# Optimization experiments

Hardware: AMD Instinct MI355X
Metric: run time of the kernel (lower is better)

The kernel has to match this reference:

```python
import jax, jax.numpy as jnp
import numpy as np

B, T, C, H, M, R = 2, 2048, 768, 6, 3072, 320
D = C // H  # head_dim = 128


def setup_inputs() -> dict:
    key = jax.random.key(0)
    ks = jax.random.split(key, 11)
    s = 0.02
    return {
        "x": jax.random.normal(ks[0], (B, T, C), jnp.float32),
        "forward_memory": jax.random.normal(ks[1], (B, M, C), jnp.float32),
        "reverse_memory": jax.random.normal(ks[2], (B, R, C), jnp.float32),
        "ctrl": jax.random.uniform(ks[3], (5,), jnp.float32),
        "Wq": jax.random.normal(ks[4], (C, C), jnp.float32) * s,
        "Wk": jax.random.normal(ks[5], (C, C), jnp.float32) * s,
        "Wv": jax.random.normal(ks[6], (C, C), jnp.float32) * s,
        "Wo": jax.random.normal(ks[7], (C, C), jnp.float32) * s,
        "Wc": jax.random.normal(ks[8], (C, 5), jnp.float32) * 1e-4,  # ctrl_init_scale
        "Wg": jax.random.normal(ks[9], (H, C), jnp.float32) * s,
        "bg": jnp.full((H,), -1.0, jnp.float32),  # gate_bias_init
    }


def reference(x, forward_memory, reverse_memory, ctrl, Wq, Wk, Wv, Wo, Wc, Wg, bg):
    Bx, Tx, Cx = x.shape
    Hx = bg.shape[0]
    Dx = Cx // Hx
    # query with control-vector fusion (ctrl broadcast to every token)
    q = x @ Wq.T + ctrl @ Wc.T  # [B,T,C]
    # concat local tokens with forward+reverse memory, project K/V once
    kv_in = jnp.concatenate([x, forward_memory, reverse_memory], axis=1)  # [B,S,C]
    k = kv_in @ Wk.T
    v = kv_in @ Wv.T

    def heads(t):
        return t.reshape(Bx, -1, Hx, Dx).transpose(0, 2, 1, 3)  # [B,H,*,D]

    qh, kh, vh = heads(q), heads(k), heads(v)
    S = kh.shape[2]
    scores = jnp.einsum("bhtd,bhsd->bhts", qh, kh) * (Dx ** -0.5)
    # causal mask over local block only; memory columns always visible
    causal = jnp.triu(jnp.ones((Tx, Tx), bool), 1)
    mask = jnp.concatenate([causal, jnp.zeros((Tx, S - Tx), bool)], axis=1)
    scores = jnp.where(mask, jnp.float32(-1e30), scores)
    w = jax.nn.softmax(scores, axis=-1)  # [B,H,T,S]
    # split attention output into local and memory contributions
    local = jnp.einsum("bhts,bhsd->bhtd", w[..., :Tx], vh[:, :, :Tx])
    mem = jnp.einsum("bhts,bhsd->bhtd", w[..., Tx:], vh[:, :, Tx:])
    # per-head sigmoid gate on the memory path, computed from the fused query
    gate = jax.nn.sigmoid(q @ Wg.T + bg)  # [B,T,H]
    gate = gate.transpose(0, 2, 1)[..., None]  # [B,H,T,1]
    out = local + gate * mem
    out = out.transpose(0, 2, 1, 3).reshape(Bx, Tx, Cx)
    return out @ Wo.T
```

## Files before the change

kernel.cpp:

```cpp
#include <hip/hip_runtime.h>


typedef unsigned short u16;
typedef unsigned int   u32;
typedef __bf16 bf16x8 __attribute__((ext_vector_type(8)));
typedef float  f32x4  __attribute__((ext_vector_type(4)));

#define B_ 2
#define T_ 2048
#define C_ 768
#define H_ 6
#define D_ 128
#define M_ 3072
#define R_ 320
#define S_ 5440
#define BT_ 4096
#define BS_ 10880
#define NS_ 3
#define NMEM_ 53

#define GLDS(src, dst) __builtin_amdgcn_global_load_lds( \
    (const __attribute__((address_space(1))) void*)(src), \
    (__attribute__((address_space(3))) void*)(dst), 16, 0, 0)

__device__ __forceinline__ float b2f(u16 u) {
  union { u32 i; float f; } c; c.i = ((u32)u) << 16; return c.f;
}
__device__ __forceinline__ u16 f2b(float f) {
  union { float f; u32 i; } c; c.f = f;
  return (u16)((c.i + 0x7FFFu + ((c.i >> 16) & 1u)) >> 16);
}

__global__ __launch_bounds__(256) void k_cast4(const float* __restrict__ s0,
                                               const float* __restrict__ s1,
                                               const float* __restrict__ s2,
                                               const float* __restrict__ s3,
                                               u16* __restrict__ d0,
                                               u16* __restrict__ d1,
                                               u16* __restrict__ d2,
                                               u16* __restrict__ d3) {
  const float* src = (blockIdx.y == 0) ? s0 : (blockIdx.y == 1) ? s1
                   : (blockIdx.y == 2) ? s2 : s3;
  u16* dst = (blockIdx.y == 0) ? d0 : (blockIdx.y == 1) ? d1
           : (blockIdx.y == 2) ? d2 : d3;
  int i = (blockIdx.x * 256 + threadIdx.x) * 4;
  float4 v = *(const float4*)(src + i);
  u16 o[4] = { f2b(v.x), f2b(v.y), f2b(v.z), f2b(v.w) };
  *(ushort4*)(dst + i) = *(ushort4*)o;
}

__global__ __launch_bounds__(256) void k_concat(const float* __restrict__ x,
                                                const float* __restrict__ fm,
                                                const float* __restrict__ rm,
                                                u16* __restrict__ kv) {
  long long i = ((long long)blockIdx.x * 256 + threadIdx.x) * 8;
  if (i >= (long long)BS_ * C_) return;
  int row = (int)(i / C_);
  int col = (int)(i - (long long)row * C_);
  int b = row / S_, s = row - b * S_;
  const float* src;
  if (s < T_)           src = x  + (size_t)(b * T_ + s) * C_ + col;
  else if (s < T_ + M_) src = fm + (size_t)(b * M_ + (s - T_)) * C_ + col;
  else                  src = rm + (size_t)(b * R_ + (s - T_ - M_)) * C_ + col;
  float4 a0 = *(const float4*)src;
  float4 a1 = *(const float4*)(src + 4);
  u16 o[8] = { f2b(a0.x), f2b(a0.y), f2b(a0.z), f2b(a0.w),
               f2b(a1.x), f2b(a1.y), f2b(a1.z), f2b(a1.w) };
  *(uint4*)(kv + i) = *(uint4*)o;
}

template<bool F32OUT, bool QCBIAS>
__global__ __launch_bounds__(256) void k_gemm(const u16* __restrict__ A,
                                              const u16* __restrict__ W,
                                              const float* __restrict__ ctrl,
                                              const float* __restrict__ Wc,
                                              void* __restrict__ outv,
                                              int rows, int rowShift, int bstride) {
  __shared__ __align__(16) u16 As[3][128 * 32];
  __shared__ __align__(16) u16 Bs[3][128 * 32];
  const int t = threadIdx.x;
  const int lane = t & 63, wv = t >> 6;
  const int wr = (wv >> 1) * 64, wc = (wv & 1) * 64;
  const int fr = lane & 15, fq = lane >> 4;
  const int rowTile = blockIdx.x * 128;
  const int colTile = blockIdx.y * 128;

  f32x4 acc[4][4] = {};

  const int e0 = t * 8;
  const int e1 = (256 + t) * 8;
  const int r0 = e0 >> 5, c0 = e0 & 31;
  const int r1 = e1 >> 5, c1 = e1 & 31;

  int gr0 = rowTile + r0; if (gr0 >= rows) gr0 = rows - 1;
  int gr1 = rowTile + r1; if (gr1 >= rows) gr1 = rows - 1;
  const int msk = (1 << rowShift) - 1;
  const size_t pr0 = (size_t)(gr0 >> rowShift) * bstride + (gr0 & msk);
  const size_t pr1 = (size_t)(gr1 >> rowShift) * bstride + (gr1 & msk);
  const u16* gaB0 = A + pr0 * C_ + c0;
  const u16* gaB1 = A + pr1 * C_ + c1;
  const u16* gbB0 = W + (size_t)(colTile + r0) * C_ + c0;
  const u16* gbB1 = W + (size_t)(colTile + r1) * C_ + c1;
  const int aOff0 = (wv * 64) * 8, aOff1 = (256 + wv * 64) * 8;

#define STAGE_G(bi, kt) do { \
    GLDS(gaB0 + (kt), &As[bi][aOff0]); \
    GLDS(gaB1 + (kt), &As[bi][aOff1]); \
    GLDS(gbB0 + (kt), &Bs[bi][aOff0]); \
    GLDS(gbB1 + (kt), &Bs[bi][aOff1]); } while (0)

  STAGE_G(0, 0);
  STAGE_G(1, 32);
  int cur = 0;

  for (int kt = 0; kt < C_; kt += 32) {
    int nx2 = cur + 2; if (nx2 >= 3) nx2 -= 3;
    if (kt + 64 < C_) {
      STAGE_G(nx2, kt + 64);
      asm volatile("s_waitcnt vmcnt(8)" ::: "memory");
    } else if (kt + 32 < C_) {
      asm volatile("s_waitcnt vmcnt(4)" ::: "memory");
    } else {
      asm volatile("s_waitcnt vmcnt(0)" ::: "memory");
    }
    __builtin_amdgcn_s_barrier();

    bf16x8 af[4], bfr[4];
#pragma unroll
    for (int i = 0; i < 4; ++i) af[i]  = *(const bf16x8*)&As[cur][(wr + i * 16 + fr) * 32 + fq * 8];
#pragma unroll
    for (int i = 0; i < 4; ++i) bfr[i] = *(const bf16x8*)&Bs[cur][(wc + i * 16 + fr) * 32 + fq * 8];
#pragma unroll
    for (int mi = 0; mi < 4; ++mi)
#pragma unroll
      for (int ni = 0; ni < 4; ++ni)
        acc[mi][ni] = __builtin_amdgcn_mfma_f32_16x16x32_bf16(af[mi], bfr[ni], acc[mi][ni], 0, 0, 0);
    __builtin_amdgcn_s_barrier();
    cur = (cur == 2) ? 0 : cur + 1;
  }
#undef STAGE_G

#pragma unroll
  for (int mi = 0; mi < 4; ++mi) {
#pragma unroll
    for (int ni = 0; ni < 4; ++ni) {
      int cc = colTile + wc + ni * 16 + fr;
      float bb = 0.f;
      if (QCBIAS) {
#pragma unroll
        for (int j = 0; j < 5; ++j) bb += ctrl[j] * Wc[cc * 5 + j];
      }
#pragma unroll
      for (int j = 0; j < 4; ++j) {
        int rr = rowTile + wr + mi * 16 + fq * 4 + j;
        if (rr < rows) {
          float val = acc[mi][ni][j] + bb;
          if (F32OUT) ((float*)outv)[(size_t)rr * C_ + cc] = val;
          else        ((u16*)outv)[(size_t)rr * C_ + cc] = f2b(val);
        }
      }
    }
  }
}

__global__ __launch_bounds__(256, 2) void k_gemmKV(const u16* __restrict__ kvb,
                                                   const u16* __restrict__ Wk,
                                                   const u16* __restrict__ Wv,
                                                   u16* __restrict__ kb,
                                                   u16* __restrict__ vt) {
  __shared__ __align__(16) u16 As[2][128 * 32];
  __shared__ __align__(16) u16 Ks2[2][128 * 32];
  __shared__ __align__(16) u16 Vs2[2][128 * 32];
  const int t = threadIdx.x;
  const int lane = t & 63, wv = t >> 6;
  const int wr = (wv >> 1) * 64, wc = (wv & 1) * 64;
  const int fr = lane & 15, fq = lane >> 4;
  const int rowTile = blockIdx.x * 128;
  const int colTile = blockIdx.y * 128;

  f32x4 accK[4][4] = {};
  f32x4 accV[4][4] = {};

  const int e0 = t * 8;
  const int e1 = (256 + t) * 8;
  const int r0 = e0 >> 5, c0 = e0 & 31;
  const int r1 = e1 >> 5, c1 = e1 & 31;

  const u16* gaB0 = kvb + (size_t)(rowTile + r0) * C_ + c0;
  const u16* gaB1 = kvb + (size_t)(rowTile + r1) * C_ + c1;
  const u16* gkB0 = Wk + (size_t)(colTile + r0) * C_ + c0;
  const u16* gkB1 = Wk + (size_t)(colTile + r1) * C_ + c1;
  const u16* gvB0 = Wv + (size_t)(colTile + r0) * C_ + c0;
  const u16* gvB1 = Wv + (size_t)(colTile + r1) * C_ + c1;
  const int aOff0 = (wv * 64) * 8, aOff1 = (256 + wv * 64) * 8;

#define STAGE_KV(bi, kt) do { \
    GLDS(gaB0 + (kt), &As[bi][aOff0]); \
    GLDS(gaB1 + (kt), &As[bi][aOff1]); \
    GLDS(gkB0 + (kt), &Ks2[bi][aOff0]); \
    GLDS(gkB1 + (kt), &Ks2[bi][aOff1]); \
    GLDS(gvB0 + (kt), &Vs2[bi][aOff0]); \
    GLDS(gvB1 + (kt), &Vs2[bi][aOff1]); } while (0)

  STAGE_KV(0, 0);
  int cur = 0;

  for (int kt = 0; kt < C_; kt += 32) {
    if (kt + 32 < C_) {
      STAGE_KV(cur ^ 1, kt + 32);
      asm volatile("s_waitcnt vmcnt(6)" ::: "memory");
    } else {
      asm volatile("s_waitcnt vmcnt(0)" ::: "memory");
    }
    __builtin_amdgcn_s_barrier();

    bf16x8 af[4], wkf[4], wvf[4];
#pragma unroll
    for (int i = 0; i < 4; ++i) af[i]  = *(const bf16x8*)&As[cur][(wr + i * 16 + fr) * 32 + fq * 8];
#pragma unroll
    for (int i = 0; i < 4; ++i) wkf[i] = *(const bf16x8*)&Ks2[cur][(wc + i * 16 + fr) * 32 + fq * 8];
#pragma unroll
    for (int i = 0; i < 4; ++i) wvf[i] = *(const bf16x8*)&Vs2[cur][(wc + i * 16 + fr) * 32 + fq * 8];
#pragma unroll
    for (int mi = 0; mi < 4; ++mi)
#pragma unroll
      for (int ni = 0; ni < 4; ++ni) {
        accK[mi][ni] = __builtin_amdgcn_mfma_f32_16x16x32_bf16(af[mi], wkf[ni], accK[mi][ni], 0, 0, 0);
        accV[mi][ni] = __builtin_amdgcn_mfma_f32_16x16x32_bf16(wvf[mi], af[ni], accV[mi][ni], 0, 0, 0);
      }
    __builtin_amdgcn_s_barrier();
    cur ^= 1;
  }
#undef STAGE_KV

#pragma unroll
  for (int mi = 0; mi < 4; ++mi) {
#pragma unroll
    for (int ni = 0; ni < 4; ++ni) {
      int cc = colTile + wc + ni * 16 + fr;
#pragma unroll
      for (int j = 0; j < 4; ++j) {
        int rr = rowTile + wr + mi * 16 + fq * 4 + j;
        kb[(size_t)rr * C_ + cc] = f2b(accK[mi][ni][j]);
      }
    }
  }
#pragma unroll
  for (int mi = 0; mi < 4; ++mi) {
#pragma unroll
    for (int ni = 0; ni < 4; ++ni) {
      int sg = rowTile + wr + ni * 16 + fr;
      int b = sg / S_, s = sg - b * S_;
#pragma unroll
      for (int j = 0; j < 4; ++j) {
        int cc = colTile + wc + mi * 16 + fq * 4 + j;
        vt[((size_t)(b * C_ + cc)) * S_ + s] = f2b(accV[mi][ni][j]);
      }
    }
  }
}

__global__ __launch_bounds__(256) void k_gate(const u16* __restrict__ q,
                                              const float* __restrict__ Wg,
                                              const float* __restrict__ bg,
                                              float* __restrict__ gate) {
  int gid = blockIdx.x * 4 + (threadIdx.x >> 6);
  int lane = threadIdx.x & 63;
  int h = gid % H_;
  int bt = gid / H_;
  const u16* qrow = q + (size_t)bt * C_;
  const float* wrow = Wg + (size_t)h * C_;
  float a = 0.f;
#pragma unroll
  for (int i = 0; i < 12; ++i) {
    int e = i * 64 + lane;
    a += b2f(qrow[e]) * wrow[e];
  }
#pragma unroll
  for (int off = 1; off < 64; off <<= 1) a += __shfl_xor(a, off);
  if (lane == 0) {
    float xg = a + bg[h];
    int b = bt / T_, tt = bt - b * T_;
    gate[((size_t)b * H_ + h) * T_ + tt] = 1.f / (1.f + __expf(-xg));
  }
}

__global__ __launch_bounds__(512, 4) void k_attn6(const u16* __restrict__ q,
                                                  const u16* __restrict__ kk,
                                                  const u16* __restrict__ vt,
                                                  const float* __restrict__ gate,
                                                  u16* __restrict__ pacc0,
                                                  u16* __restrict__ pacc1,
                                                  u16* __restrict__ pacc2,
                                                  float* __restrict__ pl) {
  __shared__ __align__(16) u16 Ks[2][64 * 128];
  __shared__ __align__(16) u16 Vs[128 * 64];
  __shared__ __align__(16) u16 Pb[8][16 * 64];

  const int bh = blockIdx.x;
  const int b = bh / H_, h = bh - b * H_;
  const int y = blockIdx.y, c = blockIdx.z;
  const int wv = threadIdx.x >> 6, lane = threadIdx.x & 63;
  const int fr = lane & 15, fq = lane >> 4;
  const int qbase = y * 128 + wv * 16;
  u16* P = Pb[wv];

  const u16* Qh = q + (size_t)(b * T_ + qbase) * C_ + h * D_;
  const float* gh = gate + ((size_t)b * H_ + h) * T_ + qbase;

  const int kRow0 = wv * 8 + (lane >> 4), kRow1 = kRow0 + 4;
  const int kCol0 = (((lane & 15) * 16) ^ ((kRow0 & 7) << 4)) >> 1;
  const int kCol1 = (((lane & 15) * 16) ^ ((kRow1 & 7) << 4)) >> 1;
  const u16* kSrc0 = kk + (size_t)(b * S_ + kRow0) * C_ + h * D_ + kCol0;
  const u16* kSrc1 = kk + (size_t)(b * S_ + kRow1) * C_ + h * D_ + kCol1;
  const int vRow0 = wv * 16 + (lane >> 3), vRow1 = vRow0 + 8;
  const int vCol0 = (((lane & 7) * 16) ^ ((vRow0 & 7) << 4)) >> 1;
  const int vCol1 = (((lane & 7) * 16) ^ ((vRow1 & 7) << 4)) >> 1;
  const u16* vSrc0 = vt + ((size_t)b * C_ + h * D_ + vRow0) * S_ + vCol0;
  const u16* vSrc1 = vt + ((size_t)b * C_ + h * D_ + vRow1) * S_ + vCol1;

  bf16x8 qf[4];
#pragma unroll
  for (int kc = 0; kc < 4; ++kc)
    qf[kc] = *(const bf16x8*)&Qh[(size_t)fr * C_ + kc * 32 + fq * 8];

  f32x4 acc[8] = {};
  f32x4 accL = {}, accM = {};
  float g4[4], lg[4];
#pragma unroll
  for (int r = 0; r < 4; ++r) { g4[r] = gh[fq * 4 + r]; lg[r] = __log2f(g4[r]); }

  const __bf16 one_h = (__bf16)1.0f;
  bf16x8 ones = { one_h, one_h, one_h, one_h, one_h, one_h, one_h, one_h };

  const float scl = 0.08838834764831845f * 1.4426950408889634f;
  const int xk = (fr & 7) << 4;

  const int nloc = 2 * y + 2;
  const int ntot = nloc + NMEM_;
  auto s_of = [&](int i) { return (i < nloc) ? i * 64 : T_ + (i - nloc) * 64; };

  {
    int s0 = s_of(c);
    GLDS(kSrc0 + (size_t)s0 * C_, &Ks[0][(wv * 8) * 128]);
    GLDS(kSrc1 + (size_t)s0 * C_, &Ks[0][(wv * 8 + 4) * 128]);
  }
  int cur = 0;

  for (int i = c; i < ntot; i += NS_) {
    const int s0 = s_of(i);
    const bool haveNext = (i + NS_ < ntot);
    GLDS(vSrc0 + s0, &Vs[(wv * 16) * 64]);
    GLDS(vSrc1 + s0, &Vs[(wv * 16 + 8) * 64]);
    if (haveNext) {
      int sn = s_of(i + NS_);
      GLDS(kSrc0 + (size_t)sn * C_, &Ks[cur ^ 1][(wv * 8) * 128]);
      GLDS(kSrc1 + (size_t)sn * C_, &Ks[cur ^ 1][(wv * 8 + 4) * 128]);
      asm volatile("s_waitcnt vmcnt(4)" ::: "memory");
    } else {
      asm volatile("s_waitcnt vmcnt(2)" ::: "memory");
    }
    __builtin_amdgcn_s_barrier();

    const bool loc = (i < nloc);
    const bool maskedStep = loc && (s0 + 63 > qbase);
    const bool skip = loc && (s0 > qbase + 15);

    bf16x8 pa0, pa1;
    if (!skip) {
      f32x4 sc[4] = {{}, {}, {}, {}};
      __builtin_amdgcn_s_setprio(1);
#pragma unroll
      for (int quad = 0; quad < 4; ++quad) {
        const u16* Krow = &Ks[cur][(quad * 16 + fr) * 128];
#pragma unroll
        for (int kc = 0; kc < 4; ++kc) {
          bf16x8 kf = *(const bf16x8*)&Krow[((kc * 64 + fq * 16) ^ xk) >> 1];
          sc[quad] = __builtin_amdgcn_mfma_f32_16x16x32_bf16(qf[kc], kf, sc[quad], 0, 0, 0);
        }
      }
      __builtin_amdgcn_s_setprio(0);
      if (maskedStep) {
#pragma unroll
        for (int quad = 0; quad < 4; ++quad)
#pragma unroll
          for (int r = 0; r < 4; ++r)
            if (s0 + quad * 16 + fr > qbase + fq * 4 + r) sc[quad][r] = -1.0e30f;
      }
      float ca[4];
#pragma unroll
      for (int r = 0; r < 4; ++r) ca[r] = loc ? 0.f : lg[r];
#pragma unroll
      for (int quad = 0; quad < 4; ++quad)
#pragma unroll
        for (int r = 0; r < 4; ++r) {
          float p = exp2f(fmaf(sc[quad][r], scl, ca[r]));
          ((__bf16*)P)[(fq * 4 + r) * 64 + quad * 16 + fr] = (__bf16)p;
        }
      __builtin_amdgcn_wave_barrier();
      pa0 = *(const bf16x8*)&P[fr * 64 + fq * 8];
      pa1 = *(const bf16x8*)&P[fr * 64 + 32 + fq * 8];
    }
    if (haveNext) asm volatile("s_waitcnt vmcnt(2)" ::: "memory");
    else          asm volatile("s_waitcnt vmcnt(0)" ::: "memory");
    __builtin_amdgcn_s_barrier();
    if (!skip) {
      __builtin_amdgcn_s_setprio(1);
#pragma unroll
      for (int nt = 0; nt < 8; ++nt) {
        const u16* Vrow = &Vs[(nt * 16 + fr) * 64];
        bf16x8 vf0 = *(const bf16x8*)&Vrow[((fq * 16) ^ xk) >> 1];
        bf16x8 vf1 = *(const bf16x8*)&Vrow[((64 + fq * 16) ^ xk) >> 1];
        acc[nt] = __builtin_amdgcn_mfma_f32_16x16x32_bf16(pa0, vf0, acc[nt], 0, 0, 0);
        acc[nt] = __builtin_amdgcn_mfma_f32_16x16x32_bf16(pa1, vf1, acc[nt], 0, 0, 0);
      }
      if (loc) {
        accL = __builtin_amdgcn_mfma_f32_16x16x32_bf16(pa0, ones, accL, 0, 0, 0);
        accL = __builtin_amdgcn_mfma_f32_16x16x32_bf16(pa1, ones, accL, 0, 0, 0);
      } else {
        accM = __builtin_amdgcn_mfma_f32_16x16x32_bf16(pa0, ones, accM, 0, 0, 0);
        accM = __builtin_amdgcn_mfma_f32_16x16x32_bf16(pa1, ones, accM, 0, 0, 0);
      }
      __builtin_amdgcn_s_setprio(0);
    }
    __builtin_amdgcn_s_barrier();
    cur ^= 1;
  }

  u16* pb = (c == 0) ? pacc0 : (c == 1) ? pacc1 : pacc2;
  const size_t rowb = (size_t)bh * T_ + qbase;
#pragma unroll
  for (int nt = 0; nt < 8; ++nt)
#pragma unroll
    for (int r = 0; r < 4; ++r)
      pb[(rowb + fq * 4 + r) * D_ + nt * 16 + fr] = f2b(acc[nt][r]);
  if (fr == 0) {
#pragma unroll
    for (int r = 0; r < 4; ++r)
      pl[((size_t)c * (B_ * H_) + bh) * T_ + qbase + fq * 4 + r] =
          accL[r] + accM[r] / g4[r];
  }
}

__global__ __launch_bounds__(256) void k_combine(const u16* __restrict__ pacc0,
                                                 const u16* __restrict__ pacc1,
                                                 const u16* __restrict__ pacc2,
                                                 const float* __restrict__ pl,
                                                 u16* __restrict__ ao) {
  const int row = blockIdx.x * 4 + (threadIdx.x >> 6);
  const int lane = threadIdx.x & 63;
  const int bh = row >> 11, t = row & (T_ - 1);
  const int b = bh / H_, h = bh - b * H_;

  float L = pl[(size_t)bh * T_ + t]
          + pl[((size_t)(B_ * H_) + bh) * T_ + t]
          + pl[((size_t)(2 * B_ * H_) + bh) * T_ + t];
  float inv = 1.f / L;
  const size_t rb = ((size_t)bh * T_ + t) * D_ + lane * 2;
  float o0 = 0.f, o1 = 0.f;
  u32 v0 = *(const u32*)&pacc0[rb];
  u32 v1 = *(const u32*)&pacc1[rb];
  u32 v2 = *(const u32*)&pacc2[rb];
  o0 = b2f((u16)(v0 & 0xFFFF)) + b2f((u16)(v1 & 0xFFFF)) + b2f((u16)(v2 & 0xFFFF));
  o1 = b2f((u16)(v0 >> 16)) + b2f((u16)(v1 >> 16)) + b2f((u16)(v2 >> 16));
  u16 o[2] = { f2b(o0 * inv), f2b(o1 * inv) };
  *(u32*)&ao[((size_t)(b * T_ + t)) * C_ + h * D_ + lane * 2] = *(u32*)o;
}

extern "C" void kernel_launch(void* const* d_in, const int* in_sizes, int n_in,
                              void* d_out, int out_size, void* d_ws, size_t ws_size,
                              hipStream_t stream) {
  const float* x   = (const float*)d_in[0];
  const float* fm  = (const float*)d_in[1];
  const float* rm  = (const float*)d_in[2];
  const float* ctl = (const float*)d_in[3];
  const float* Wq  = (const float*)d_in[4];
  const float* Wk  = (const float*)d_in[5];
  const float* Wv  = (const float*)d_in[6];
  const float* Wo  = (const float*)d_in[7];
  const float* Wc  = (const float*)d_in[8];
  const float* Wg  = (const float*)d_in[9];
  const float* bg  = (const float*)d_in[10];
  float* outp = (float*)d_out;

  char* ws = (char*)d_ws;
  float* gate = (float*)(ws + 4096);
  u16* qb    = (u16*)(ws + 102400);
  u16* kv    = (u16*)(ws + 6393856);
  u16* pacc0 = (u16*)(ws + 6393856);
  u16* pacc1 = (u16*)(ws + 12685312);
  u16* kb    = (u16*)(ws + 23105536);
  u16* vt    = (u16*)(ws + 39817216);
  u16* ao    = (u16*)(ws + 39817216);
  u16* pacc2 = (u16*)(ws + 56528896);
  float* pl  = (float*)(ws + 62820352);
  u16* Wqb   = (u16*)(ws + 63115264);
  u16* Wkb   = (u16*)(ws + 64294912);
  u16* Wvb   = (u16*)(ws + 65474560);
  u16* Wob   = (u16*)(ws + 66654208);

  k_cast4<<<dim3(576, 4), dim3(256), 0, stream>>>(Wq, Wk, Wv, Wo,
                                                  Wqb, Wkb, Wvb, Wob);
  k_concat<<<dim3(4080), dim3(256), 0, stream>>>(x, fm, rm, kv);
  k_gemm<false, true><<<dim3(32, 6), dim3(256), 0, stream>>>(
      kv, Wqb, ctl, Wc, qb, BT_, 11, S_);
  k_gemmKV<<<dim3(85, 6), dim3(256), 0, stream>>>(kv, Wkb, Wvb, kb, vt);
  k_gate<<<dim3(6144), dim3(256), 0, stream>>>(qb, Wg, bg, gate);
  k_attn6<<<dim3(B_ * H_, 16, NS_), dim3(512), 0, stream>>>(
      qb, kb, vt, gate, pacc0, pacc1, pacc2, pl);
  k_combine<<<dim3(6144), dim3(256), 0, stream>>>(pacc0, pacc1, pacc2, pl, ao);
  k_gemm<true, false><<<dim3(32, 6), dim3(256), 0, stream>>>(
      ao, Wob, nullptr, nullptr, outp, BT_, 30, 0);
}
```

Measured before the change: 217.1 us.

## Raise attention split count, reuse K buffer for P, reverse tile order

The attention kernel now splits the key range four ways instead of three, adding a fourth partial accumulator buffer that the combine kernel also reads. The dedicated P staging buffer is dropped: P is written with a swizzle into the K slot that was just consumed, after the barrier, which cuts LDS use so the launch bound can ask for 6 blocks per CU. Query tiles run in reverse order so the heavier causal tiles start first, and the setprio hints are removed. The trade-offs are more combine traffic and extra partial-sum storage, and holding the exp'd scores in registers across the barrier raises register pressure.

Result: slower. 451.0 us (+107.8%).

```diff
diff --git a/kernel.cpp b/kernel.cpp
--- a/kernel.cpp
+++ b/kernel.cpp
@@ -16,7 +16,7 @@
 #define S_ 5440
 #define BT_ 4096
 #define BS_ 10880
-#define NS_ 3
+#define NS_ 4
 #define NMEM_ 53
 
 #define GLDS(src, dst) __builtin_amdgcn_global_load_lds( \
@@ -285,25 +285,25 @@
   }
 }
 
-__global__ __launch_bounds__(512, 4) void k_attn6(const u16* __restrict__ q,
+__global__ __launch_bounds__(512, 6) void k_attn7(const u16* __restrict__ q,
                                                   const u16* __restrict__ kk,
                                                   const u16* __restrict__ vt,
                                                   const float* __restrict__ gate,
                                                   u16* __restrict__ pacc0,
                                                   u16* __restrict__ pacc1,
                                                   u16* __restrict__ pacc2,
+                                                  u16* __restrict__ pacc3,
                                                   float* __restrict__ pl) {
   __shared__ __align__(16) u16 Ks[2][64 * 128];
   __shared__ __align__(16) u16 Vs[128 * 64];
-  __shared__ __align__(16) u16 Pb[8][16 * 64];
 
   const int bh = blockIdx.x;
   const int b = bh / H_, h = bh - b * H_;
-  const int y = blockIdx.y, c = blockIdx.z;
+  const int y = 15 - blockIdx.y;
+  const int c = blockIdx.z;
   const int wv = threadIdx.x >> 6, lane = threadIdx.x & 63;
   const int fr = lane & 15, fq = lane >> 4;
   const int qbase = y * 128 + wv * 16;
-  u16* P = Pb[wv];
 
   const u16* Qh = q + (size_t)(b * T_ + qbase) * C_ + h * D_;
   const float* gh = gate + ((size_t)b * H_ + h) * T_ + qbase;
@@ -366,10 +366,8 @@
     const bool maskedStep = loc && (s0 + 63 > qbase);
     const bool skip = loc && (s0 > qbase + 15);
 
-    bf16x8 pa0, pa1;
+    f32x4 sc[4] = {{}, {}, {}, {}};
     if (!skip) {
-      f32x4 sc[4] = {{}, {}, {}, {}};
-      __builtin_amdgcn_s_setprio(1);
 #pragma unroll
       for (int quad = 0; quad < 4; ++quad) {
         const u16* Krow = &Ks[cur][(quad * 16 + fr) * 128];
@@ -379,7 +377,6 @@
           sc[quad] = __builtin_amdgcn_mfma_f32_16x16x32_bf16(qf[kc], kf, sc[quad], 0, 0, 0);
         }
       }
-      __builtin_amdgcn_s_setprio(0);
       if (maskedStep) {
 #pragma unroll
         for (int quad = 0; quad < 4; ++quad)
@@ -393,19 +390,25 @@
 #pragma unroll
       for (int quad = 0; quad < 4; ++quad)
 #pragma unroll
+        for (int r = 0; r < 4; ++r)
+          sc[quad][r] = exp2f(fmaf(sc[quad][r], scl, ca[r]));
+    }
+    if (haveNext) asm volatile("s_waitcnt vmcnt(2)" ::: "memory");
+    else          asm volatile("s_waitcnt vmcnt(0)" ::: "memory");
+    __builtin_amdgcn_s_barrier();
+    if (!skip) {
+      char* Pc = (char*)&Ks[cur][wv * 1024];
+#pragma unroll
+      for (int quad = 0; quad < 4; ++quad)
+#pragma unroll
         for (int r = 0; r < 4; ++r) {
-          float p = exp2f(fmaf(sc[quad][r], scl, ca[r]));
-          ((__bf16*)P)[(fq * 4 + r) * 64 + quad * 16 + fr] = (__bf16)p;
+          int row = fq * 4 + r;
+          int cb = (quad * 32 + fr * 2) ^ ((row & 7) << 4);
+          *(u16*)(Pc + row * 128 + cb) = f2b(sc[quad][r]);
         }
       __builtin_amdgcn_wave_barrier();
-      pa0 = *(const bf16x8*)&P[fr * 64 + fq * 8];
-      pa1 = *(const bf16x8*)&P[fr * 64 + 32 + fq * 8];
-    }
-    if (haveNext) asm volatile("s_waitcnt vmcnt(2)" ::: "memory");
-    else          asm volatile("s_waitcnt vmcnt(0)" ::: "memory");
-    __builtin_amdgcn_s_barrier();
-    if (!skip) {
-      __builtin_amdgcn_s_setprio(1);
+      bf16x8 pa0 = *(const bf16x8*)(Pc + fr * 128 + ((fq * 16) ^ ((fr & 7) << 4)));
+      bf16x8 pa1 = *(const bf16x8*)(Pc + fr * 128 + ((64 + fq * 16) ^ ((fr & 7) << 4)));
 #pragma unroll
       for (int nt = 0; nt < 8; ++nt) {
         const u16* Vrow = &Vs[(nt * 16 + fr) * 64];
@@ -421,13 +424,12 @@
         accM = __builtin_amdgcn_mfma_f32_16x16x32_bf16(pa0, ones, accM, 0, 0, 0);
         accM = __builtin_amdgcn_mfma_f32_16x16x32_bf16(pa1, ones, accM, 0, 0, 0);
       }
-      __builtin_amdgcn_s_setprio(0);
     }
     __builtin_amdgcn_s_barrier();
     cur ^= 1;
   }
 
-  u16* pb = (c == 0) ? pacc0 : (c == 1) ? pacc1 : pacc2;
+  u16* pb = (c == 0) ? pacc0 : (c == 1) ? pacc1 : (c == 2) ? pacc2 : pacc3;
   const size_t rowb = (size_t)bh * T_ + qbase;
 #pragma unroll
   for (int nt = 0; nt < 8; ++nt)
@@ -445,6 +447,7 @@
 __global__ __launch_bounds__(256) void k_combine(const u16* __restrict__ pacc0,
                                                  const u16* __restrict__ pacc1,
                                                  const u16* __restrict__ pacc2,
+                                                 const u16* __restrict__ pacc3,
                                                  const float* __restrict__ pl,
                                                  u16* __restrict__ ao) {
   const int row = blockIdx.x * 4 + (threadIdx.x >> 6);
@@ -454,15 +457,18 @@
 
   float L = pl[(size_t)bh * T_ + t]
           + pl[((size_t)(B_ * H_) + bh) * T_ + t]
-          + pl[((size_t)(2 * B_ * H_) + bh) * T_ + t];
+          + pl[((size_t)(2 * B_ * H_) + bh) * T_ + t]
+          + pl[((size_t)(3 * B_ * H_) + bh) * T_ + t];
   float inv = 1.f / L;
   const size_t rb = ((size_t)bh * T_ + t) * D_ + lane * 2;
-  float o0 = 0.f, o1 = 0.f;
   u32 v0 = *(const u32*)&pacc0[rb];
   u32 v1 = *(const u32*)&pacc1[rb];
   u32 v2 = *(const u32*)&pacc2[rb];
-  o0 = b2f((u16)(v0 & 0xFFFF)) + b2f((u16)(v1 & 0xFFFF)) + b2f((u16)(v2 & 0xFFFF));
-  o1 = b2f((u16)(v0 >> 16)) + b2f((u16)(v1 >> 16)) + b2f((u16)(v2 >> 16));
+  u32 v3 = *(const u32*)&pacc3[rb];
+  float o0 = b2f((u16)(v0 & 0xFFFF)) + b2f((u16)(v1 & 0xFFFF))
+           + b2f((u16)(v2 & 0xFFFF)) + b2f((u16)(v3 & 0xFFFF));
+  float o1 = b2f((u16)(v0 >> 16)) + b2f((u16)(v1 >> 16))
+           + b2f((u16)(v2 >> 16)) + b2f((u16)(v3 >> 16));
   u16 o[2] = { f2b(o0 * inv), f2b(o1 * inv) };
   *(u32*)&ao[((size_t)(b * T_ + t)) * C_ + h * D_ + lane * 2] = *(u32*)o;
 }
@@ -493,11 +499,12 @@
   u16* vt    = (u16*)(ws + 39817216);
   u16* ao    = (u16*)(ws + 39817216);
   u16* pacc2 = (u16*)(ws + 56528896);
-  float* pl  = (float*)(ws + 62820352);
-  u16* Wqb   = (u16*)(ws + 63115264);
-  u16* Wkb   = (u16*)(ws + 64294912);
-  u16* Wvb   = (u16*)(ws + 65474560);
-  u16* Wob   = (u16*)(ws + 66654208);
+  u16* pacc3 = (u16*)(ws + 62820352);
+  float* pl  = (float*)(ws + 69111808);
+  u16* Wqb   = (u16*)(ws + 69505024);
+  u16* Wkb   = (u16*)(ws + 70684672);
+  u16* Wvb   = (u16*)(ws + 71864320);
+  u16* Wob   = (u16*)(ws + 73043968);
 
   k_cast4<<<dim3(576, 4), dim3(256), 0, stream>>>(Wq, Wk, Wv, Wo,
                                                   Wqb, Wkb, Wvb, Wob);
@@ -506,9 +513,9 @@
       kv, Wqb, ctl, Wc, qb, BT_, 11, S_);
   k_gemmKV<<<dim3(85, 6), dim3(256), 0, stream>>>(kv, Wkb, Wvb, kb, vt);
   k_gate<<<dim3(6144), dim3(256), 0, stream>>>(qb, Wg, bg, gate);
-  k_attn6<<<dim3(B_ * H_, 16, NS_), dim3(512), 0, stream>>>(
-      qb, kb, vt, gate, pacc0, pacc1, pacc2, pl);
-  k_combine<<<dim3(6144), dim3(256), 0, stream>>>(pacc0, pacc1, pacc2, pl, ao);
+  k_attn7<<<dim3(B_ * H_, 16, NS_), dim3(512), 0, stream>>>(
+      qb, kb, vt, gate, pacc0, pacc1, pacc2, pacc3, pl);
+  k_combine<<<dim3(6144), dim3(256), 0, stream>>>(pacc0, pacc1, pacc2, pacc3, pl, ao);
   k_gemm<true, false><<<dim3(32, 6), dim3(256), 0, stream>>>(
       ao, Wob, nullptr, nullptr, outp, BT_, 30, 0);
 }
```
